# Optimization experiments

Measured on AMD Instinct MI355X. Metric: run time of the kernel, lower is better.

Reference implementation:

```python
import jax, jax.numpy as jnp
from jax import lax
import numpy as np

# dims
B, T, W, D = 8, 24, 48, 512
H = 8            # n_head
E = D // H       # head dim = 64
DI = 2 * D       # mamba d_inner (expand=2) = 1024
S = 64           # d_state
R = 32           # dt_rank = ceil(512/16)
KC = 4           # mamba depthwise conv kernel
DFF = 2048       # ffn hidden
L = T * W


def setup_inputs() -> dict:
    key = jax.random.key(0)
    ks = jax.random.split(key, 32)
    def g(i, shape, s=0.02):
        return jax.random.normal(ks[i], shape, dtype=jnp.float32) * s
    inp = {
        "x": jax.random.normal(ks[0], (B, T, W, D), dtype=jnp.float32),
        "slf_attn_mask": jnp.zeros((B, L), dtype=bool),
        # attention projections (torch Linear convention: y = x @ W.T + b)
        "Wq": g(1, (D, D)), "bq": jnp.zeros((D,), jnp.float32),
        "Wk": g(2, (D, D)), "bk": jnp.zeros((D,), jnp.float32),
        "Wv": g(3, (D, D)), "bv": jnp.zeros((D,), jnp.float32),
        "Wo": g(4, (D, D)), "bo": jnp.zeros((D,), jnp.float32),
        # mamba params
        "in_proj_w": g(5, (2 * DI, D)),
        "conv_w": g(6, (DI, KC), 0.1),
        "conv_b": jnp.zeros((DI,), jnp.float32),
        "x_proj_w": g(7, (R + 2 * S, DI)),
        "dt_proj_w": g(8, (DI, R), 0.1),
        "dt_proj_b": jnp.full((DI,), -3.0, jnp.float32),  # softplus -> small dt
        "A_log": jnp.broadcast_to(jnp.log(jnp.arange(1, S + 1, dtype=jnp.float32)), (DI, S)).copy(),
        "D_ssm": jnp.ones((DI,), jnp.float32),
        "out_proj_w": g(9, (D, DI)),
        # hybrid LayerNorm
        "ln1_g": jnp.ones((D,), jnp.float32), "ln1_b": jnp.zeros((D,), jnp.float32),
        # FFN (pre-norm)
        "ffn_w1": g(10, (DFF, D)), "ffn_b1": jnp.zeros((DFF,), jnp.float32),
        "ffn_w2": g(11, (D, DFF)), "ffn_b2": jnp.zeros((D,), jnp.float32),
        "ln2_g": jnp.ones((D,), jnp.float32), "ln2_b": jnp.zeros((D,), jnp.float32),
    }
    return inp


def _layernorm(x, g, b, eps):
    m = jnp.mean(x, -1, keepdims=True)
    v = jnp.mean(jnp.square(x - m), -1, keepdims=True)
    return (x - m) * lax.rsqrt(v + eps) * g + b


def _attention(xf, mask, Wq, bq, Wk, bk, Wv, bv, Wo, bo):
    # xf: [B, L, D]; mask: [B, L] bool (True = masked)
    b, l, _ = xf.shape
    q = (xf @ Wq.T + bq).reshape(b, l, H, E)
    k = (xf @ Wk.T + bk).reshape(b, l, H, E)
    v = (xf @ Wv.T + bv).reshape(b, l, H, E)
    scale = 1.0 / jnp.sqrt(jnp.float32(E))
    scores = jnp.einsum('blhe,bshe->bhls', q, k)                 # [B,H,L,L]
    scores = jnp.where(mask[:, None, None, :], -jnp.inf, scores)
    probs = jax.nn.softmax(scale * scores, axis=-1)
    out = jnp.einsum('bhls,bshe->blhe', probs, v).reshape(b, l, D)
    return out @ Wo.T + bo


def _mamba(xf, in_proj_w, conv_w, conv_b, x_proj_w, dt_proj_w, dt_proj_b, A_log, D_ssm, out_proj_w):
    # xf: [B, L, D]
    b, l, _ = xf.shape
    xz = xf @ in_proj_w.T                  # [B,L,2*DI]
    u, z = jnp.split(xz, 2, axis=-1)
    # causal depthwise conv1d, kernel KC
    up = jnp.pad(u, ((0, 0), (KC - 1, 0), (0, 0)))
    uc = conv_b + sum(up[:, k:k + l, :] * conv_w[:, k] for k in range(KC))
    u = jax.nn.silu(uc)                    # [B,L,DI]
    xdbc = u @ x_proj_w.T                  # [B,L,R+2S]
    dt_r, Bm, Cm = jnp.split(xdbc, [R, R + S], axis=-1)
    delta = jax.nn.softplus(dt_r @ dt_proj_w.T + dt_proj_b)   # [B,L,DI]
    A = -jnp.exp(A_log)                    # [DI,S]

    def step(h, xs):
        dt_t, u_t, B_t, C_t = xs           # [B,DI],[B,DI],[B,S],[B,S]
        dA = jnp.exp(dt_t[:, :, None] * A)                       # [B,DI,S]
        h = h * dA + (dt_t * u_t)[:, :, None] * B_t[:, None, :]
        y = jnp.einsum('bds,bs->bd', h, C_t)
        return h, y

    xs = (delta.transpose(1, 0, 2), u.transpose(1, 0, 2),
          Bm.transpose(1, 0, 2), Cm.transpose(1, 0, 2))
    h0 = jnp.zeros((b, DI, S), dtype=xf.dtype)
    _, ys = lax.scan(step, h0, xs)
    y = ys.transpose(1, 0, 2) + u * D_ssm  # [B,L,DI]
    y = y * jax.nn.silu(z)
    return y @ out_proj_w.T


def _forward(x, slf_attn_mask, Wq, bq, Wk, bk, Wv, bv, Wo, bo,
             in_proj_w, conv_w, conv_b, x_proj_w, dt_proj_w, dt_proj_b,
             A_log, D_ssm, out_proj_w, ln1_g, ln1_b,
             ffn_w1, ffn_b1, ffn_w2, ffn_b2, ln2_g, ln2_b):
    b, t, w, d = x.shape
    xf = x.reshape(b, t * w, d)
    x_attn = _attention(xf, slf_attn_mask, Wq, bq, Wk, bk, Wv, bv, Wo, bo)
    x_mamba = _mamba(xf, in_proj_w, conv_w, conv_b, x_proj_w, dt_proj_w,
                     dt_proj_b, A_log, D_ssm, out_proj_w)
    h = xf + x_attn + x_mamba
    h = _layernorm(h, ln1_g, ln1_b, 1e-5)
    # pre-norm FFN with residual
    hn = _layernorm(h, ln2_g, ln2_b, 1e-6)
    ff = jax.nn.gelu(hn @ ffn_w1.T + ffn_b1, approximate=False) @ ffn_w2.T + ffn_b2
    out = h + ff
    return out.reshape(b, t, w, d)


def reference(x, slf_attn_mask, Wq, bq, Wk, bk, Wv, bv, Wo, bo,
              in_proj_w, conv_w, conv_b, x_proj_w, dt_proj_w, dt_proj_b,
              A_log, D_ssm, out_proj_w, ln1_g, ln1_b,
              ffn_w1, ffn_b1, ffn_w2, ffn_b2, ln2_g, ln2_b):
    return _forward(x, slf_attn_mask, Wq, bq, Wk, bk, Wv, bv, Wo, bo,
                    in_proj_w, conv_w, conv_b, x_proj_w, dt_proj_w, dt_proj_b,
                    A_log, D_ssm, out_proj_w, ln1_g, ln1_b,
                    ffn_w1, ffn_b1, ffn_w2, ffn_b2, ln2_g, ln2_b)
```

## Files before the change

### kernel.cpp

```cpp
#include <hip/hip_runtime.h>
#include <hip/hip_bf16.h>
#include <math.h>

#define BB 8
#define DD 512
#define HH 8
#define EE 64
#define DI 1024
#define SS 64
#define RR 32
#define KCONV 4
#define DFF 2048
#define LL 1152
#define ML (BB*LL)
#define XS (RR + 2*SS)

typedef short bf16x8 __attribute__((ext_vector_type(8)));
typedef float f32x4 __attribute__((ext_vector_type(4)));
typedef unsigned short u16x4 __attribute__((ext_vector_type(4)));

#define GLD_LDS(g, l) \
  __builtin_amdgcn_global_load_lds((const __attribute__((address_space(1))) void*)(g), \
                                   (__attribute__((address_space(3))) void*)(l), 16, 0, 0)

__device__ __forceinline__ float bf2f(unsigned short u) {
  return __uint_as_float(((unsigned)u) << 16);
}

template<int IMM>
__device__ __forceinline__ float swz(float x) {
  return __uint_as_float((unsigned)__builtin_amdgcn_ds_swizzle((int)__float_as_uint(x), IMM));
}

__global__ __launch_bounds__(256) void cvt_bf16(
    const float* __restrict__ s, __hip_bfloat16* __restrict__ d, int n)
{
  const int i = (blockIdx.x * 256 + threadIdx.x) * 4;
  if (i + 3 < n) {
    const float4 v = *(const float4*)(s + i);
    __hip_bfloat16 t[4] = {__float2bfloat16(v.x), __float2bfloat16(v.y),
                           __float2bfloat16(v.z), __float2bfloat16(v.w)};
    *(ushort4*)(d + i) = *(const ushort4*)t;
  } else {
    for (int k = i; k < n; ++k) d[k] = __float2bfloat16(s[k]);
  }
}

__global__ __launch_bounds__(256) void gemm_mfma(
    const __hip_bfloat16* __restrict__ A, int lda,
    const __hip_bfloat16* __restrict__ W,
    const float* __restrict__ bias,
    const float* __restrict__ res,
    void* __restrict__ Cv,
    int M, int N, int K, int act, int mode)
{
  __shared__ __align__(16) __hip_bfloat16 As[128 * 32];
  __shared__ __align__(16) __hip_bfloat16 Ws[128 * 32];
  const int tid = threadIdx.x;
  const int wid = tid >> 6, lane = tid & 63;
  const int wr = wid >> 1, wc = wid & 1;
  const int m0 = blockIdx.y << 7, n0 = blockIdx.x << 7;
  const int r1 = tid >> 2;
  const int c1 = (tid & 3) << 3;

  const __hip_bfloat16* ga0 = A + (size_t)(m0 + r1) * lda + c1;
  const __hip_bfloat16* ga1 = A + (size_t)(m0 + 64 + r1) * lda + c1;
  const __hip_bfloat16* gw0 = W + (size_t)(n0 + r1) * K + c1;
  const __hip_bfloat16* gw1 = W + (size_t)(n0 + 64 + r1) * K + c1;
  char* lA0 = (char*)As + wid * 1024;
  char* lA1 = lA0 + 4096;
  char* lW0 = (char*)Ws + wid * 1024;
  char* lW1 = lW0 + 4096;

  f32x4 acc[4][4];
#pragma unroll
  for (int i = 0; i < 4; ++i)
#pragma unroll
    for (int j = 0; j < 4; ++j) acc[i][j] = (f32x4){0.f, 0.f, 0.f, 0.f};

  const int fm = lane & 15;
  const int q8 = (lane >> 4) << 3;

  for (int kt = 0; kt < K; kt += 32) {
    __syncthreads();
    GLD_LDS(ga0, lA0); GLD_LDS(ga1, lA1);
    GLD_LDS(gw0, lW0); GLD_LDS(gw1, lW1);
    ga0 += 32; ga1 += 32; gw0 += 32; gw1 += 32;
    __syncthreads();

    bf16x8 af[4], wf[4];
#pragma unroll
    for (int i = 0; i < 4; ++i)
      af[i] = *(const bf16x8*)((const short*)As + (wr * 64 + i * 16 + fm) * 32 + q8);
#pragma unroll
    for (int j = 0; j < 4; ++j)
      wf[j] = *(const bf16x8*)((const short*)Ws + (wc * 64 + j * 16 + fm) * 32 + q8);
#pragma unroll
    for (int i = 0; i < 4; ++i)
#pragma unroll
      for (int j = 0; j < 4; ++j)
        acc[i][j] = __builtin_amdgcn_mfma_f32_16x16x32_bf16(af[i], wf[j], acc[i][j], 0, 0, 0);
  }

  const int rquad = (lane >> 4) << 2;
#pragma unroll
  for (int j = 0; j < 4; ++j) {
    const int n = n0 + wc * 64 + j * 16 + fm;
    if (n < N) {
      const float bv = bias ? bias[n] : 0.f;
#pragma unroll
      for (int i = 0; i < 4; ++i) {
        const int mb = m0 + wr * 64 + i * 16 + rquad;
#pragma unroll
        for (int r = 0; r < 4; ++r) {
          const int m = mb + r;
          float v = acc[i][j][r] + bv;
          if (act == 1) v = 0.5f * v * (1.f + erff(v * 0.70710678118654752f));
          else if (act == 2) v = fmaxf(v, 0.f) + log1pf(expf(-fabsf(v)));
          if (mode == 2) {
            const int bb2 = m / LL;
            const int key = m - bb2 * LL;
            ((__hip_bfloat16*)Cv)[((size_t)(bb2 * HH + (n >> 6)) * EE + (n & 63)) * LL + key] =
                __float2bfloat16(v);
          } else {
            const size_t off = (size_t)m * N + n;
            if (res) v += res[off];
            if (mode == 1) ((__hip_bfloat16*)Cv)[off] = __float2bfloat16(v);
            else ((float*)Cv)[off] = v;
          }
        }
      }
    }
  }
}

__global__ __launch_bounds__(256) void conv_silu(
    const __hip_bfloat16* __restrict__ upre, const float* __restrict__ cw,
    const float* __restrict__ cb, __hip_bfloat16* __restrict__ uout)
{
  const size_t idx = (size_t)blockIdx.x * 256 + threadIdx.x;
  if (idx >= (size_t)ML * DI) return;
  const int di = (int)(idx & (DI - 1));
  const int t = (int)((idx >> 10) % LL);
  float acc = cb[di];
#pragma unroll
  for (int k = 0; k < KCONV; ++k) {
    if (t - (KCONV - 1) + k >= 0)
      acc = fmaf((float)upre[idx - (size_t)(KCONV - 1 - k) * DI], cw[di * KCONV + k], acc);
  }
  uout[idx] = __float2bfloat16(acc / (1.f + __expf(-acc)));
}

#define SLOAD(P, t0) { _Pragma("unroll") for (int j = 0; j < 4; ++j) { \
    P##_dt[j] = dp[(size_t)((t0)+j)*DI]; \
    P##_u[j]  = bf2f(ubp[(size_t)((t0)+j)*DI]); \
    P##_B[j]  = *(const u16x4*)(Bp + (size_t)((t0)+j)*XS); \
    P##_C[j]  = *(const u16x4*)(Cp + (size_t)((t0)+j)*XS); } }

#define SSTEP(P, j, t) { \
    const float dtu = P##_dt[j] * P##_u[j]; \
    h0 = fmaf(h0, __expf(P##_dt[j] * Av[0]), dtu * bf2f(P##_B[j][0])); \
    h1 = fmaf(h1, __expf(P##_dt[j] * Av[1]), dtu * bf2f(P##_B[j][1])); \
    h2 = fmaf(h2, __expf(P##_dt[j] * Av[2]), dtu * bf2f(P##_B[j][2])); \
    h3 = fmaf(h3, __expf(P##_dt[j] * Av[3]), dtu * bf2f(P##_B[j][3])); \
    float part = h0 * bf2f(P##_C[j][0]); \
    part = fmaf(h1, bf2f(P##_C[j][1]), part); \
    part = fmaf(h2, bf2f(P##_C[j][2]), part); \
    part = fmaf(h3, bf2f(P##_C[j][3]), part); \
    part += swz<0x041F>(part); part += swz<0x081F>(part); \
    part += swz<0x101F>(part); part += swz<0x201F>(part); \
    ystash = (((t) & 15) == s4) ? part : ystash; }

#define SCOMP(P, t0) { _Pragma("unroll") for (int j = 0; j < 4; ++j) SSTEP(P, j, (t0)+j) }

__global__ __launch_bounds__(256) void scan_kernel(
    const float* __restrict__ delta, const __hip_bfloat16* __restrict__ ubf,
    const __hip_bfloat16* __restrict__ zbf, const __hip_bfloat16* __restrict__ xdbc,
    const float* __restrict__ A_log, const float* __restrict__ D_ssm,
    __hip_bfloat16* __restrict__ y)
{
  const int wv = (int)((blockIdx.x * 256 + threadIdx.x) >> 6);
  const int lane = threadIdx.x & 63;
  const int c = lane >> 4;
  const int s4 = lane & 15;
  const int g = (wv << 2) + c;
  const int b = g >> 10;
  const int di = g & (DI - 1);
  float Av[4];
#pragma unroll
  for (int kk = 0; kk < 4; ++kk)
    Av[kk] = -__expf(A_log[di * SS + (s4 << 2) + kk]);
  const float Dd = D_ssm[di];
  const size_t rb = (size_t)b * LL;
  const float* __restrict__ dp = delta + rb * DI + di;
  const unsigned short* __restrict__ ubp = (const unsigned short*)ubf + rb * DI + di;
  const unsigned short* __restrict__ zbp = (const unsigned short*)zbf + rb * DI + di;
  const unsigned short* __restrict__ Bp = (const unsigned short*)xdbc + rb * XS + RR + (s4 << 2);
  const unsigned short* __restrict__ Cp = Bp + SS;
  __hip_bfloat16* __restrict__ yp = y + rb * DI + di;

  float h0 = 0.f, h1 = 0.f, h2 = 0.f, h3 = 0.f;
  float ystash = 0.f;
  float a_dt[4], a_u[4]; u16x4 a_B[4], a_C[4];
  float b_dt[4], b_u[4]; u16x4 b_B[4], b_C[4];

  SLOAD(a, 0)
  for (int t0 = 0; t0 < LL; t0 += 8) {
    SLOAD(b, t0 + 4)
    SCOMP(a, t0)
    if (t0 + 8 < LL) SLOAD(a, t0 + 8)
    SCOMP(b, t0 + 4)
    if (((t0 + 8) & 15) == 0) {
      const int tf = t0 - 8 + s4;
      const float uv = bf2f(ubp[(size_t)tf * DI]);
      const float zv = bf2f(zbp[(size_t)tf * DI]);
      const float yv = (ystash + uv * Dd) * (zv / (1.f + __expf(-zv)));
      yp[(size_t)tf * DI] = __float2bfloat16(yv);
      ystash = 0.f;
    }
  }
}

__global__ __launch_bounds__(256) void attn_mfma(
    const __hip_bfloat16* __restrict__ qg, const __hip_bfloat16* __restrict__ kg,
    const __hip_bfloat16* __restrict__ vtg, __hip_bfloat16* __restrict__ og)
{
  __shared__ __align__(16) __hip_bfloat16 Qs[64][72];
  __shared__ __align__(16) __hip_bfloat16 Ks[64][72];
  __shared__ __align__(16) __hip_bfloat16 Vts[64][72];
  __shared__ __align__(16) __hip_bfloat16 Ps[4][16][72];
  const int tid = threadIdx.x;
  const int w = tid >> 6, lane = tid & 63;
  const int bh = blockIdx.y;
  const int b = bh >> 3, hh = bh & 7;
  const int q0 = blockIdx.x << 6;
  const size_t qkbase = (size_t)b * LL * DD + (size_t)hh * EE;
  const size_t vtbase = (size_t)bh * EE * LL;

  const int srow = tid >> 2, sch = (tid & 3) << 4;
  {
    const __hip_bfloat16* src = qg + qkbase + (size_t)(q0 + srow) * DD + sch;
    *(uint4*)&Qs[srow][sch]     = *(const uint4*)src;
    *(uint4*)&Qs[srow][sch + 8] = *(const uint4*)(src + 8);
  }
  __syncthreads();

  const int fm = lane & 15;
  const int q8 = (lane >> 4) << 3;
  bf16x8 af0 = *(const bf16x8*)&Qs[w * 16 + fm][q8];
  bf16x8 af1 = *(const bf16x8*)&Qs[w * 16 + fm][32 + q8];

  f32x4 oacc[4];
  float m_i[4], l_i[4];
#pragma unroll
  for (int r = 0; r < 4; ++r) { m_i[r] = -INFINITY; l_i[r] = 0.f; }
#pragma unroll
  for (int j = 0; j < 4; ++j) oacc[j] = (f32x4){0.f, 0.f, 0.f, 0.f};

  for (int kt = 0; kt < LL / 64; ++kt) {
    const int k0 = kt << 6;
    __syncthreads();
    {
      const __hip_bfloat16* ksrc = kg + qkbase + (size_t)(k0 + srow) * DD + sch;
      const __hip_bfloat16* vsrc = vtg + vtbase + (size_t)srow * LL + k0 + sch;
      *(uint4*)&Ks[srow][sch]      = *(const uint4*)ksrc;
      *(uint4*)&Ks[srow][sch + 8]  = *(const uint4*)(ksrc + 8);
      *(uint4*)&Vts[srow][sch]     = *(const uint4*)vsrc;
      *(uint4*)&Vts[srow][sch + 8] = *(const uint4*)(vsrc + 8);
    }
    __syncthreads();

    f32x4 sacc[4];
#pragma unroll
    for (int j = 0; j < 4; ++j) sacc[j] = (f32x4){0.f, 0.f, 0.f, 0.f};
#pragma unroll
    for (int j = 0; j < 4; ++j) {
      bf16x8 kf0 = *(const bf16x8*)&Ks[j * 16 + fm][q8];
      bf16x8 kf1 = *(const bf16x8*)&Ks[j * 16 + fm][32 + q8];
      sacc[j] = __builtin_amdgcn_mfma_f32_16x16x32_bf16(af0, kf0, sacc[j], 0, 0, 0);
      sacc[j] = __builtin_amdgcn_mfma_f32_16x16x32_bf16(af1, kf1, sacc[j], 0, 0, 0);
    }

    float alpha[4];
#pragma unroll
    for (int r = 0; r < 4; ++r) {
#pragma unroll
      for (int j = 0; j < 4; ++j) sacc[j][r] *= 0.125f;
      float mt = fmaxf(fmaxf(sacc[0][r], sacc[1][r]), fmaxf(sacc[2][r], sacc[3][r]));
      mt = fmaxf(mt, swz<0x041F>(mt)); mt = fmaxf(mt, swz<0x081F>(mt));
      mt = fmaxf(mt, swz<0x101F>(mt)); mt = fmaxf(mt, swz<0x201F>(mt));
      const float mn = fmaxf(m_i[r], mt);
      alpha[r] = __expf(m_i[r] - mn);
      m_i[r] = mn;
      float p[4], rs = 0.f;
#pragma unroll
      for (int j = 0; j < 4; ++j) { p[j] = __expf(sacc[j][r] - mn); rs += p[j]; }
      rs += swz<0x041F>(rs); rs += swz<0x081F>(rs);
      rs += swz<0x101F>(rs); rs += swz<0x201F>(rs);
      l_i[r] = l_i[r] * alpha[r] + rs;
      const int qrow = ((lane >> 4) << 2) + r;
#pragma unroll
      for (int j = 0; j < 4; ++j)
        Ps[w][qrow][j * 16 + fm] = __float2bfloat16(p[j]);
    }
#pragma unroll
    for (int j = 0; j < 4; ++j)
#pragma unroll
      for (int r = 0; r < 4; ++r) oacc[j][r] *= alpha[r];

    bf16x8 pf0 = *(const bf16x8*)&Ps[w][fm][q8];
    bf16x8 pf1 = *(const bf16x8*)&Ps[w][fm][32 + q8];
#pragma unroll
    for (int j = 0; j < 4; ++j) {
      bf16x8 v0 = *(const bf16x8*)&Vts[j * 16 + fm][q8];
      bf16x8 v1 = *(const bf16x8*)&Vts[j * 16 + fm][32 + q8];
      oacc[j] = __builtin_amdgcn_mfma_f32_16x16x32_bf16(pf0, v0, oacc[j], 0, 0, 0);
      oacc[j] = __builtin_amdgcn_mfma_f32_16x16x32_bf16(pf1, v1, oacc[j], 0, 0, 0);
    }
  }

#pragma unroll
  for (int r = 0; r < 4; ++r) {
    const float inv = 1.f / l_i[r];
    const int qq = q0 + w * 16 + ((lane >> 4) << 2) + r;
#pragma unroll
    for (int j = 0; j < 4; ++j)
      og[qkbase + (size_t)qq * DD + j * 16 + fm] = __float2bfloat16(oacc[j][r] * inv);
  }
}

__device__ __forceinline__ float block_sum512(float val, float* sm)
{
#pragma unroll
  for (int off = 32; off; off >>= 1) val += __shfl_xor(val, off, 64);
  const int wid = threadIdx.x >> 6;
  __syncthreads();
  if ((threadIdx.x & 63) == 0) sm[wid] = val;
  __syncthreads();
  return sm[0] + sm[1] + sm[2] + sm[3];
}

__global__ __launch_bounds__(256) void ln_fused(
    const float* __restrict__ xf, const float* __restrict__ ao,
    const float* __restrict__ mo,
    const float* __restrict__ g1, const float* __restrict__ b1,
    const float* __restrict__ g2, const float* __restrict__ b2,
    float* __restrict__ hout, __hip_bfloat16* __restrict__ hnout)
{
  __shared__ float sm[4];
  const size_t base = (size_t)blockIdx.x * DD;
  const int t = threadIdx.x;
  const float v0 = xf[base + t] + ao[base + t] + mo[base + t];
  const float v1 = xf[base + 256 + t] + ao[base + 256 + t] + mo[base + 256 + t];
  const float mean = block_sum512(v0 + v1, sm) * (1.f / DD);
  const float d0 = v0 - mean, d1 = v1 - mean;
  const float var = block_sum512(d0 * d0 + d1 * d1, sm) * (1.f / DD);
  const float rstd = rsqrtf(var + 1e-5f);
  const float h0 = d0 * rstd * g1[t] + b1[t];
  const float h1 = d1 * rstd * g1[t + 256] + b1[t + 256];
  hout[base + t] = h0;
  hout[base + 256 + t] = h1;
  const float mean2 = block_sum512(h0 + h1, sm) * (1.f / DD);
  const float e0 = h0 - mean2, e1 = h1 - mean2;
  const float var2 = block_sum512(e0 * e0 + e1 * e1, sm) * (1.f / DD);
  const float rstd2 = rsqrtf(var2 + 1e-6f);
  hnout[base + t] = __float2bfloat16(e0 * rstd2 * g2[t] + b2[t]);
  hnout[base + 256 + t] = __float2bfloat16(e1 * rstd2 * g2[t + 256] + b2[t + 256]);
}

extern "C" void kernel_launch(void* const* d_in, const int* in_sizes, int n_in,
                              void* d_out, int out_size, void* d_ws, size_t ws_size,
                              hipStream_t stream)
{
  const float* x         = (const float*)d_in[0];
  const float* Wq        = (const float*)d_in[2];
  const float* bq        = (const float*)d_in[3];
  const float* Wk        = (const float*)d_in[4];
  const float* bk        = (const float*)d_in[5];
  const float* Wv        = (const float*)d_in[6];
  const float* bv        = (const float*)d_in[7];
  const float* Wo        = (const float*)d_in[8];
  const float* bo        = (const float*)d_in[9];
  const float* in_proj_w = (const float*)d_in[10];
  const float* conv_w    = (const float*)d_in[11];
  const float* conv_b    = (const float*)d_in[12];
  const float* x_proj_w  = (const float*)d_in[13];
  const float* dt_proj_w = (const float*)d_in[14];
  const float* dt_proj_b = (const float*)d_in[15];
  const float* A_log     = (const float*)d_in[16];
  const float* D_ssm     = (const float*)d_in[17];
  const float* out_proj_w= (const float*)d_in[18];
  const float* ln1_g     = (const float*)d_in[19];
  const float* ln1_b     = (const float*)d_in[20];
  const float* ffn_w1    = (const float*)d_in[21];
  const float* ffn_b1    = (const float*)d_in[22];
  const float* ffn_w2    = (const float*)d_in[23];
  const float* ffn_b2    = (const float*)d_in[24];
  const float* ln2_g     = (const float*)d_in[25];
  const float* ln2_b     = (const float*)d_in[26];
  float* out = (float*)d_out;

  float* ws = (float*)d_ws;
  const size_t OF_XBF = 2506752;
  const size_t OF_UQ  = 4866048;
  const size_t OF_ZV  = 9584640;
  const size_t OF_UH  = 14303232;
  const size_t OF_XD  = 19021824;
  const size_t OF_DF  = 19759104;
  const size_t OF_YA  = 29196288;

  __hip_bfloat16* wbf     = (__hip_bfloat16*)ws;
  __hip_bfloat16* xbf     = (__hip_bfloat16*)(ws + OF_XBF);
  __hip_bfloat16* upre_bf = (__hip_bfloat16*)(ws + OF_UQ);
  __hip_bfloat16* qbf     = upre_bf;
  __hip_bfloat16* kbf     = upre_bf + (size_t)ML * DD;
  __hip_bfloat16* z_bf    = (__hip_bfloat16*)(ws + OF_ZV);
  __hip_bfloat16* vtbf    = z_bf;
  __hip_bfloat16* ubf     = (__hip_bfloat16*)(ws + OF_UH);
  float*          hbuf    = ws + OF_UH;
  __hip_bfloat16* xdbc_bf = (__hip_bfloat16*)(ws + OF_XD);
  float*          deltab  = ws + OF_DF;
  float*          mambab  = deltab;
  float*          aobuf   = deltab + (size_t)ML * DD;
  __hip_bfloat16* ffbf    = (__hip_bfloat16*)(ws + OF_DF);
  __hip_bfloat16* ybf     = (__hip_bfloat16*)(ws + OF_YA);
  __hip_bfloat16* attnbf  = ybf;
  __hip_bfloat16* hnbf    = (__hip_bfloat16*)(ws + OF_YA + 2359296);

  const size_t w_inproj = 0;
  const size_t w_xproj  = 1048576;
  const size_t w_dt     = 1310720;
  const size_t w_out    = 1343488;
  const size_t w_q      = 1867776;
  const size_t w_k      = 2129920;
  const size_t w_v      = 2392064;
  const size_t w_o      = 2654208;
  const size_t w_f1     = 2916352;
  const size_t w_f2     = 3964928;

  const dim3 thr(256);
#define CVT(src, dst, n) cvt_bf16<<<dim3(((n)/4 + 255)/256), thr, 0, stream>>>(src, dst, n)
#define GEMM(Abf, lda_, Woff, Bptr, Rptr, Cptr, N_, K_, act_, md_) \
  gemm_mfma<<<dim3((N_ + 127)/128, ML/128), thr, 0, stream>>>( \
      Abf, lda_, wbf + (Woff), Bptr, Rptr, (void*)(Cptr), ML, N_, K_, act_, md_)

  hipMemsetAsync((void*)(wbf + w_xproj + (size_t)160 * 1024), 0, (size_t)96 * 1024 * 2, stream);
  CVT(in_proj_w, wbf + w_inproj, 1048576);
  CVT(x_proj_w,  wbf + w_xproj,  163840);
  CVT(dt_proj_w, wbf + w_dt,     32768);
  CVT(out_proj_w,wbf + w_out,    524288);
  CVT(Wq,        wbf + w_q,      262144);
  CVT(Wk,        wbf + w_k,      262144);
  CVT(Wv,        wbf + w_v,      262144);
  CVT(Wo,        wbf + w_o,      262144);
  CVT(ffn_w1,    wbf + w_f1,     1048576);
  CVT(ffn_w2,    wbf + w_f2,     1048576);
  CVT(x,         xbf,            ML * DD);

  GEMM(xbf, DD, w_inproj,          nullptr, nullptr, upre_bf, DI, DD, 0, 1);
  GEMM(xbf, DD, w_inproj + 524288, nullptr, nullptr, z_bf,    DI, DD, 0, 1);
  conv_silu<<<dim3((ML * DI) / 256), thr, 0, stream>>>(upre_bf, conv_w, conv_b, ubf);
  GEMM(ubf, DI, w_xproj,           nullptr, nullptr, xdbc_bf, XS, DI, 0, 1);
  GEMM(xdbc_bf, XS, w_dt,          dt_proj_b, nullptr, deltab, DI, RR, 2, 0);
  scan_kernel<<<dim3(512), thr, 0, stream>>>(
      deltab, ubf, z_bf, xdbc_bf, A_log, D_ssm, ybf);
  GEMM(ybf, DI, w_out,             nullptr, nullptr, mambab, DD, DI, 0, 0);

  GEMM(xbf, DD, w_q, bq, nullptr, qbf,  DD, DD, 0, 1);
  GEMM(xbf, DD, w_k, bk, nullptr, kbf,  DD, DD, 0, 1);
  GEMM(xbf, DD, w_v, bv, nullptr, vtbf, DD, DD, 0, 2);
  attn_mfma<<<dim3(LL / 64, BB * HH), thr, 0, stream>>>(qbf, kbf, vtbf, attnbf);
  GEMM(attnbf, DD, w_o, bo, nullptr, aobuf, DD, DD, 0, 0);

  ln_fused<<<dim3(ML), thr, 0, stream>>>(x, aobuf, mambab, ln1_g, ln1_b,
                                         ln2_g, ln2_b, hbuf, hnbf);

  GEMM(hnbf, DD, w_f1, ffn_b1, nullptr, ffbf, DFF, DD, 1, 1);
  GEMM(ffbf, DFF, w_f2, ffn_b2, hbuf, out, DD, DFF, 0, 0);
#undef GEMM
#undef CVT
}
```

Before: 1.111 ms.

## Merge in_proj and QKV GEMMs, batch scan output reduction via transpose-sum

The two in_proj GEMMs (x and z halves) become one N=2048 GEMM writing an interleaved xz buffer. The Q/K/V projections become one N=1536 GEMM with concatenated weights and bias, where a new epilogue mode writes Q|K row-major and V transposed. The scan kernel now processes 16 timesteps per iteration and combines their partial sums in one butterfly transpose-reduction, replacing four swizzles per step. This cuts kernel launches, reuses the A tile across more output columns, and lowers cross-lane shuffle work in the scan, at the cost of more registers in the scan and a reshuffled workspace layout.

After: 1.042 ms. 6.2% less time.

```diff
diff --git a/kernel.cpp b/kernel.cpp
--- a/kernel.cpp
+++ b/kernel.cpp
@@ -14,6 +14,7 @@
 #define LL 1152
 #define ML (BB*LL)
 #define XS (RR + 2*SS)
+#define ZSTR 2048
 
 typedef short bf16x8 __attribute__((ext_vector_type(8)));
 typedef float f32x4 __attribute__((ext_vector_type(4)));
@@ -51,7 +52,7 @@
     const __hip_bfloat16* __restrict__ W,
     const float* __restrict__ bias,
     const float* __restrict__ res,
-    void* __restrict__ Cv,
+    void* __restrict__ Cv, void* __restrict__ Cv2,
     int M, int N, int K, int act, int mode)
 {
   __shared__ __align__(16) __hip_bfloat16 As[128 * 32];
@@ -117,11 +118,16 @@
           float v = acc[i][j][r] + bv;
           if (act == 1) v = 0.5f * v * (1.f + erff(v * 0.70710678118654752f));
           else if (act == 2) v = fmaxf(v, 0.f) + log1pf(expf(-fabsf(v)));
-          if (mode == 2) {
-            const int bb2 = m / LL;
-            const int key = m - bb2 * LL;
-            ((__hip_bfloat16*)Cv)[((size_t)(bb2 * HH + (n >> 6)) * EE + (n & 63)) * LL + key] =
-                __float2bfloat16(v);
+          if (mode == 3) {
+            if (n < 1024) {
+              ((__hip_bfloat16*)Cv)[(size_t)m * 1024 + n] = __float2bfloat16(v);
+            } else {
+              const int e = n - 1024;
+              const int bb2 = m / LL;
+              const int key = m - bb2 * LL;
+              ((__hip_bfloat16*)Cv2)[((size_t)(bb2 * HH + (e >> 6)) * EE + (e & 63)) * LL + key] =
+                  __float2bfloat16(v);
+            }
           } else {
             const size_t off = (size_t)m * N + n;
             if (res) v += res[off];
@@ -135,47 +141,49 @@
 }
 
 __global__ __launch_bounds__(256) void conv_silu(
-    const __hip_bfloat16* __restrict__ upre, const float* __restrict__ cw,
+    const __hip_bfloat16* __restrict__ xz, const float* __restrict__ cw,
     const float* __restrict__ cb, __hip_bfloat16* __restrict__ uout)
 {
   const size_t idx = (size_t)blockIdx.x * 256 + threadIdx.x;
   if (idx >= (size_t)ML * DI) return;
   const int di = (int)(idx & (DI - 1));
-  const int t = (int)((idx >> 10) % LL);
+  const int row = (int)(idx >> 10);
+  const int t = row % LL;
   float acc = cb[di];
 #pragma unroll
   for (int k = 0; k < KCONV; ++k) {
     if (t - (KCONV - 1) + k >= 0)
-      acc = fmaf((float)upre[idx - (size_t)(KCONV - 1 - k) * DI], cw[di * KCONV + k], acc);
+      acc = fmaf((float)xz[(size_t)(row - (KCONV - 1 - k)) * ZSTR + di],
+                 cw[di * KCONV + k], acc);
   }
   uout[idx] = __float2bfloat16(acc / (1.f + __expf(-acc)));
 }
 
-#define SLOAD(P, t0) { _Pragma("unroll") for (int j = 0; j < 4; ++j) { \
-    P##_dt[j] = dp[(size_t)((t0)+j)*DI]; \
-    P##_u[j]  = bf2f(ubp[(size_t)((t0)+j)*DI]); \
-    P##_B[j]  = *(const u16x4*)(Bp + (size_t)((t0)+j)*XS); \
-    P##_C[j]  = *(const u16x4*)(Cp + (size_t)((t0)+j)*XS); } }
-
-#define SSTEP(P, j, t) { \
-    const float dtu = P##_dt[j] * P##_u[j]; \
-    h0 = fmaf(h0, __expf(P##_dt[j] * Av[0]), dtu * bf2f(P##_B[j][0])); \
-    h1 = fmaf(h1, __expf(P##_dt[j] * Av[1]), dtu * bf2f(P##_B[j][1])); \
-    h2 = fmaf(h2, __expf(P##_dt[j] * Av[2]), dtu * bf2f(P##_B[j][2])); \
-    h3 = fmaf(h3, __expf(P##_dt[j] * Av[3]), dtu * bf2f(P##_B[j][3])); \
-    float part = h0 * bf2f(P##_C[j][0]); \
-    part = fmaf(h1, bf2f(P##_C[j][1]), part); \
-    part = fmaf(h2, bf2f(P##_C[j][2]), part); \
-    part = fmaf(h3, bf2f(P##_C[j][3]), part); \
-    part += swz<0x041F>(part); part += swz<0x081F>(part); \
-    part += swz<0x101F>(part); part += swz<0x201F>(part); \
-    ystash = (((t) & 15) == s4) ? part : ystash; }
-
-#define SCOMP(P, t0) { _Pragma("unroll") for (int j = 0; j < 4; ++j) SSTEP(P, j, (t0)+j) }
+#define SLOAD(P_, t0_) { _Pragma("unroll") for (int j = 0; j < 4; ++j) { \
+    P_##_dt[j] = dp[(size_t)((t0_)+j)*DI]; \
+    P_##_u[j]  = bf2f(ubp[(size_t)((t0_)+j)*DI]); \
+    P_##_B[j]  = *(const u16x4*)(Bp + (size_t)((t0_)+j)*XS); \
+    P_##_C[j]  = *(const u16x4*)(Cp + (size_t)((t0_)+j)*XS); } }
+
+#define SSTEP(P_, j, idx) { \
+    const float dtu = P_##_dt[j] * P_##_u[j]; \
+    h0 = fmaf(h0, __expf(P_##_dt[j] * Av[0]), dtu * bf2f(P_##_B[j][0])); \
+    h1 = fmaf(h1, __expf(P_##_dt[j] * Av[1]), dtu * bf2f(P_##_B[j][1])); \
+    h2 = fmaf(h2, __expf(P_##_dt[j] * Av[2]), dtu * bf2f(P_##_B[j][2])); \
+    h3 = fmaf(h3, __expf(P_##_dt[j] * Av[3]), dtu * bf2f(P_##_B[j][3])); \
+    float part = h0 * bf2f(P_##_C[j][0]); \
+    part = fmaf(h1, bf2f(P_##_C[j][1]), part); \
+    part = fmaf(h2, bf2f(P_##_C[j][2]), part); \
+    part = fmaf(h3, bf2f(P_##_C[j][3]), part); \
+    Pp[(idx)] = part; }
+
+#define SCOMP(P_, base_) { \
+    SSTEP(P_, 0, (base_)+0) SSTEP(P_, 1, (base_)+1) \
+    SSTEP(P_, 2, (base_)+2) SSTEP(P_, 3, (base_)+3) }
 
 __global__ __launch_bounds__(256) void scan_kernel(
     const float* __restrict__ delta, const __hip_bfloat16* __restrict__ ubf,
-    const __hip_bfloat16* __restrict__ zbf, const __hip_bfloat16* __restrict__ xdbc,
+    const __hip_bfloat16* __restrict__ xz, const __hip_bfloat16* __restrict__ xdbc,
     const float* __restrict__ A_log, const float* __restrict__ D_ssm,
     __hip_bfloat16* __restrict__ y)
 {
@@ -194,35 +202,69 @@
   const size_t rb = (size_t)b * LL;
   const float* __restrict__ dp = delta + rb * DI + di;
   const unsigned short* __restrict__ ubp = (const unsigned short*)ubf + rb * DI + di;
-  const unsigned short* __restrict__ zbp = (const unsigned short*)zbf + rb * DI + di;
+  const unsigned short* __restrict__ zbp = (const unsigned short*)xz + rb * ZSTR + DI + di;
   const unsigned short* __restrict__ Bp = (const unsigned short*)xdbc + rb * XS + RR + (s4 << 2);
   const unsigned short* __restrict__ Cp = Bp + SS;
   __hip_bfloat16* __restrict__ yp = y + rb * DI + di;
 
   float h0 = 0.f, h1 = 0.f, h2 = 0.f, h3 = 0.f;
-  float ystash = 0.f;
+  float Pp[16];
   float a_dt[4], a_u[4]; u16x4 a_B[4], a_C[4];
   float b_dt[4], b_u[4]; u16x4 b_B[4], b_C[4];
-
-  SLOAD(a, 0)
-  for (int t0 = 0; t0 < LL; t0 += 8) {
-    SLOAD(b, t0 + 4)
-    SCOMP(a, t0)
-    if (t0 + 8 < LL) SLOAD(a, t0 + 8)
-    SCOMP(b, t0 + 4)
-    if (((t0 + 8) & 15) == 0) {
-      const int tf = t0 - 8 + s4;
-      const float uv = bf2f(ubp[(size_t)tf * DI]);
-      const float zv = bf2f(zbp[(size_t)tf * DI]);
-      const float yv = (ystash + uv * Dd) * (zv / (1.f + __expf(-zv)));
-      yp[(size_t)tf * DI] = __float2bfloat16(yv);
-      ystash = 0.f;
-    }
+  float c_dt[4], c_u[4]; u16x4 c_B[4], c_C[4];
+  float d_dt[4], d_u[4]; u16x4 d_B[4], d_C[4];
+
+  float u_e = bf2f(ubp[(size_t)s4 * DI]);
+  float z_e = bf2f(zbp[(size_t)s4 * ZSTR]);
+
+  SLOAD(a, 0) SLOAD(b, 4) SLOAD(c, 8)
+  for (int t0 = 0; t0 < LL; t0 += 16) {
+    SLOAD(d, t0 + 12)
+    SCOMP(a, 0)
+    if (t0 + 16 < LL) SLOAD(a, t0 + 16)
+    SCOMP(b, 4)
+    float u_n = 0.f, z_n = 0.f;
+    if (t0 + 16 < LL) {
+      u_n = bf2f(ubp[(size_t)(t0 + 16 + s4) * DI]);
+      z_n = bf2f(zbp[(size_t)(t0 + 16 + s4) * ZSTR]);
+    }
+    if (t0 + 20 < LL) SLOAD(b, t0 + 20)
+    SCOMP(c, 8)
+    if (t0 + 24 < LL) SLOAD(c, t0 + 24)
+    SCOMP(d, 12)
+
+#pragma unroll
+    for (int k2 = 0; k2 < 8; ++k2) {
+      const float mn = (s4 & 1) ? Pp[2*k2+1] : Pp[2*k2];
+      const float ot = (s4 & 1) ? Pp[2*k2]   : Pp[2*k2+1];
+      Pp[k2] = mn + swz<0x041F>(ot);
+    }
+#pragma unroll
+    for (int k2 = 0; k2 < 4; ++k2) {
+      const float mn = (s4 & 2) ? Pp[2*k2+1] : Pp[2*k2];
+      const float ot = (s4 & 2) ? Pp[2*k2]   : Pp[2*k2+1];
+      Pp[k2] = mn + swz<0x081F>(ot);
+    }
+#pragma unroll
+    for (int k2 = 0; k2 < 2; ++k2) {
+      const float mn = (s4 & 4) ? Pp[2*k2+1] : Pp[2*k2];
+      const float ot = (s4 & 4) ? Pp[2*k2]   : Pp[2*k2+1];
+      Pp[k2] = mn + swz<0x101F>(ot);
+    }
+    {
+      const float mn = (s4 & 8) ? Pp[1] : Pp[0];
+      const float ot = (s4 & 8) ? Pp[0] : Pp[1];
+      Pp[0] = mn + swz<0x201F>(ot);
+    }
+
+    const float yv = (Pp[0] + u_e * Dd) * (z_e / (1.f + __expf(-z_e)));
+    yp[(size_t)(t0 + s4) * DI] = __float2bfloat16(yv);
+    u_e = u_n; z_e = z_n;
   }
 }
 
 __global__ __launch_bounds__(256) void attn_mfma(
-    const __hip_bfloat16* __restrict__ qg, const __hip_bfloat16* __restrict__ kg,
+    const __hip_bfloat16* __restrict__ qk,
     const __hip_bfloat16* __restrict__ vtg, __hip_bfloat16* __restrict__ og)
 {
   __shared__ __align__(16) __hip_bfloat16 Qs[64][72];
@@ -234,12 +276,13 @@
   const int bh = blockIdx.y;
   const int b = bh >> 3, hh = bh & 7;
   const int q0 = blockIdx.x << 6;
-  const size_t qkbase = (size_t)b * LL * DD + (size_t)hh * EE;
+  const size_t qbase = (size_t)b * LL * 1024 + (size_t)hh * EE;
   const size_t vtbase = (size_t)bh * EE * LL;
+  const size_t obase = (size_t)b * LL * DD + (size_t)hh * EE;
 
   const int srow = tid >> 2, sch = (tid & 3) << 4;
   {
-    const __hip_bfloat16* src = qg + qkbase + (size_t)(q0 + srow) * DD + sch;
+    const __hip_bfloat16* src = qk + qbase + (size_t)(q0 + srow) * 1024 + sch;
     *(uint4*)&Qs[srow][sch]     = *(const uint4*)src;
     *(uint4*)&Qs[srow][sch + 8] = *(const uint4*)(src + 8);
   }
@@ -261,7 +304,7 @@
     const int k0 = kt << 6;
     __syncthreads();
     {
-      const __hip_bfloat16* ksrc = kg + qkbase + (size_t)(k0 + srow) * DD + sch;
+      const __hip_bfloat16* ksrc = qk + qbase + 512 + (size_t)(k0 + srow) * 1024 + sch;
       const __hip_bfloat16* vsrc = vtg + vtbase + (size_t)srow * LL + k0 + sch;
       *(uint4*)&Ks[srow][sch]      = *(const uint4*)ksrc;
       *(uint4*)&Ks[srow][sch + 8]  = *(const uint4*)(ksrc + 8);
@@ -325,7 +368,7 @@
     const int qq = q0 + w * 16 + ((lane >> 4) << 2) + r;
 #pragma unroll
     for (int j = 0; j < 4; ++j)
-      og[qkbase + (size_t)qq * DD + j * 16 + fm] = __float2bfloat16(oacc[j][r] * inv);
+      og[obase + (size_t)qq * DD + j * 16 + fm] = __float2bfloat16(oacc[j][r] * inv);
   }
 }
 
@@ -402,81 +445,78 @@
 
   float* ws = (float*)d_ws;
   const size_t OF_XBF = 2506752;
-  const size_t OF_UQ  = 4866048;
-  const size_t OF_ZV  = 9584640;
-  const size_t OF_UH  = 14303232;
-  const size_t OF_XD  = 19021824;
-  const size_t OF_DF  = 19759104;
-  const size_t OF_YA  = 29196288;
+  const size_t OF_XZ  = OF_XBF + 2359296;
+  const size_t OF_UBF = OF_XZ + 9437184;
+  const size_t OF_XD  = OF_UBF + 4718592;
+  const size_t OF_DF  = OF_XD + 737280;
+  const size_t OF_YB  = OF_DF + 9437184;
+  const size_t OF_QB  = OF_YB + 4718592;
 
   __hip_bfloat16* wbf     = (__hip_bfloat16*)ws;
   __hip_bfloat16* xbf     = (__hip_bfloat16*)(ws + OF_XBF);
-  __hip_bfloat16* upre_bf = (__hip_bfloat16*)(ws + OF_UQ);
-  __hip_bfloat16* qbf     = upre_bf;
-  __hip_bfloat16* kbf     = upre_bf + (size_t)ML * DD;
-  __hip_bfloat16* z_bf    = (__hip_bfloat16*)(ws + OF_ZV);
-  __hip_bfloat16* vtbf    = z_bf;
-  __hip_bfloat16* ubf     = (__hip_bfloat16*)(ws + OF_UH);
-  float*          hbuf    = ws + OF_UH;
+  __hip_bfloat16* hnbf    = (__hip_bfloat16*)(ws + OF_XBF);
+  __hip_bfloat16* xz      = (__hip_bfloat16*)(ws + OF_XZ);
+  __hip_bfloat16* qkbuf   = (__hip_bfloat16*)(ws + OF_XZ);
+  __hip_bfloat16* vtbf    = (__hip_bfloat16*)(ws + OF_XZ + 4718592);
+  __hip_bfloat16* ubf     = (__hip_bfloat16*)(ws + OF_UBF);
+  float*          aobuf   = ws + OF_UBF;
   __hip_bfloat16* xdbc_bf = (__hip_bfloat16*)(ws + OF_XD);
   float*          deltab  = ws + OF_DF;
-  float*          mambab  = deltab;
-  float*          aobuf   = deltab + (size_t)ML * DD;
+  __hip_bfloat16* attnbf  = (__hip_bfloat16*)(ws + OF_DF);
+  float*          mambab  = ws + OF_DF + 2359296;
   __hip_bfloat16* ffbf    = (__hip_bfloat16*)(ws + OF_DF);
-  __hip_bfloat16* ybf     = (__hip_bfloat16*)(ws + OF_YA);
-  __hip_bfloat16* attnbf  = ybf;
-  __hip_bfloat16* hnbf    = (__hip_bfloat16*)(ws + OF_YA + 2359296);
+  __hip_bfloat16* ybf     = (__hip_bfloat16*)(ws + OF_YB);
+  float*          hbuf    = ws + OF_YB;
+  float*          qkvbias = ws + OF_QB;
 
   const size_t w_inproj = 0;
   const size_t w_xproj  = 1048576;
   const size_t w_dt     = 1310720;
   const size_t w_out    = 1343488;
   const size_t w_q      = 1867776;
-  const size_t w_k      = 2129920;
-  const size_t w_v      = 2392064;
   const size_t w_o      = 2654208;
   const size_t w_f1     = 2916352;
   const size_t w_f2     = 3964928;
 
   const dim3 thr(256);
 #define CVT(src, dst, n) cvt_bf16<<<dim3(((n)/4 + 255)/256), thr, 0, stream>>>(src, dst, n)
-#define GEMM(Abf, lda_, Woff, Bptr, Rptr, Cptr, N_, K_, act_, md_) \
+#define GEMM(Abf, lda_, Woff, Bptr, Rptr, Cptr, C2ptr, N_, K_, act_, md_) \
   gemm_mfma<<<dim3((N_ + 127)/128, ML/128), thr, 0, stream>>>( \
-      Abf, lda_, wbf + (Woff), Bptr, Rptr, (void*)(Cptr), ML, N_, K_, act_, md_)
+      Abf, lda_, wbf + (Woff), Bptr, Rptr, (void*)(Cptr), (void*)(C2ptr), ML, N_, K_, act_, md_)
 
   hipMemsetAsync((void*)(wbf + w_xproj + (size_t)160 * 1024), 0, (size_t)96 * 1024 * 2, stream);
   CVT(in_proj_w, wbf + w_inproj, 1048576);
   CVT(x_proj_w,  wbf + w_xproj,  163840);
   CVT(dt_proj_w, wbf + w_dt,     32768);
   CVT(out_proj_w,wbf + w_out,    524288);
-  CVT(Wq,        wbf + w_q,      262144);
-  CVT(Wk,        wbf + w_k,      262144);
-  CVT(Wv,        wbf + w_v,      262144);
+  CVT(Wq,        wbf + w_q,           262144);
+  CVT(Wk,        wbf + w_q + 262144,  262144);
+  CVT(Wv,        wbf + w_q + 524288,  262144);
   CVT(Wo,        wbf + w_o,      262144);
   CVT(ffn_w1,    wbf + w_f1,     1048576);
   CVT(ffn_w2,    wbf + w_f2,     1048576);
   CVT(x,         xbf,            ML * DD);
-
-  GEMM(xbf, DD, w_inproj,          nullptr, nullptr, upre_bf, DI, DD, 0, 1);
-  GEMM(xbf, DD, w_inproj + 524288, nullptr, nullptr, z_bf,    DI, DD, 0, 1);
-  conv_silu<<<dim3((ML * DI) / 256), thr, 0, stream>>>(upre_bf, conv_w, conv_b, ubf);
-  GEMM(ubf, DI, w_xproj,           nullptr, nullptr, xdbc_bf, XS, DI, 0, 1);
-  GEMM(xdbc_bf, XS, w_dt,          dt_proj_b, nullptr, deltab, DI, RR, 2, 0);
+  hipMemcpyAsync(qkvbias,        bq, 512 * sizeof(float), hipMemcpyDeviceToDevice, stream);
+  hipMemcpyAsync(qkvbias + 512,  bk, 512 * sizeof(float), hipMemcpyDeviceToDevice, stream);
+  hipMemcpyAsync(qkvbias + 1024, bv, 512 * sizeof(float), hipMemcpyDeviceToDevice, stream);
+
+  GEMM(xbf, DD, w_inproj, nullptr, nullptr, xz, nullptr, 2 * DI, DD, 0, 1);
+  conv_silu<<<dim3((ML * DI) / 256), thr, 0, stream>>>(xz, conv_w, conv_b, ubf);
+  GEMM(ubf, DI, w_xproj, nullptr, nullptr, xdbc_bf, nullptr, XS, DI, 0, 1);
+  GEMM(xdbc_bf, XS, w_dt, dt_proj_b, nullptr, deltab, nullptr, DI, RR, 2, 0);
   scan_kernel<<<dim3(512), thr, 0, stream>>>(
-      deltab, ubf, z_bf, xdbc_bf, A_log, D_ssm, ybf);
-  GEMM(ybf, DI, w_out,             nullptr, nullptr, mambab, DD, DI, 0, 0);
-
-  GEMM(xbf, DD, w_q, bq, nullptr, qbf,  DD, DD, 0, 1);
-  GEMM(xbf, DD, w_k, bk, nullptr, kbf,  DD, DD, 0, 1);
-  GEMM(xbf, DD, w_v, bv, nullptr, vtbf, DD, DD, 0, 2);
-  attn_mfma<<<dim3(LL / 64, BB * HH), thr, 0, stream>>>(qbf, kbf, vtbf, attnbf);
-  GEMM(attnbf, DD, w_o, bo, nullptr, aobuf, DD, DD, 0, 0);
+      deltab, ubf, xz, xdbc_bf, A_log, D_ssm, ybf);
+  GEMM(ybf, DI, w_out, nullptr, nullptr, mambab, nullptr, DD, DI, 0, 0);
+
+  GEMM(xbf, DD, w_q, qkvbias, nullptr, qkbuf, vtbf, 3 * DD, DD, 0, 3);
+  attn_mfma<<<dim3(LL / 64, BB * HH), thr, 0, stream>>>(qkbuf, vtbf, attnbf);
+  GEMM(attnbf, DD, w_o, bo, nullptr, aobuf, nullptr, DD, DD, 0, 0);
 
   ln_fused<<<dim3(ML), thr, 0, stream>>>(x, aobuf, mambab, ln1_g, ln1_b,
                                          ln2_g, ln2_b, hbuf, hnbf);
 
-  GEMM(hnbf, DD, w_f1, ffn_b1, nullptr, ffbf, DFF, DD, 1, 1);
-  GEMM(ffbf, DFF, w_f2, ffn_b2, hbuf, out, DD, DFF, 0, 0);
+  GEMM(hnbf, DD, w_f1, ffn_b1, nullptr, ffbf, nullptr, DFF, DD, 1, 1);
+  GEMM(ffbf, DFF, w_f2, ffn_b2, hbuf, out, nullptr, DD, DFF, 0, 0);
 #undef GEMM
 #undef CVT
 }
```
